# Kernel tuning notes

Measured on AMD Instinct MI355X. Metric: run time of the kernel, lower is better.

The kernel has to match this reference:

```python
import jax, jax.numpy as jnp
import numpy as np

N, M, B, C, L, H = 8192, 8192, 16, 512, 64, 8
HEAD_DIM = C // H
PER_BATCH_KEYS = M // B
MASK_VAL = -1000.0  # matches torch masked_fill_ value


def setup_inputs() -> dict:
    key0 = jax.random.key(0)
    ks = jax.random.split(key0, 8)
    query = jax.random.normal(ks[0], (N, C), jnp.float32)
    key = jax.random.normal(ks[1], (M, C), jnp.float32)
    value = jax.random.normal(ks[2], (M, C), jnp.float32)
    # xavier-ish init for projections
    in_proj_weight = jax.random.normal(ks[3], (3 * C, C), jnp.float32) * (1.0 / np.sqrt(C))
    in_proj_bias = jnp.zeros((3 * C,), jnp.float32)
    out_w = jax.random.normal(ks[4], (C, C), jnp.float32) * (1.0 / np.sqrt(C))
    out_b = jnp.zeros((C,), jnp.float32)
    index_pair = jax.random.randint(ks[5], (N, L), 0, PER_BATCH_KEYS).astype(jnp.int32)
    pad = jax.random.uniform(ks[6], (N, L)) < 0.05
    index_pair = jnp.where(pad, jnp.int32(-1), index_pair)
    query_batch_cnt = jnp.full((B,), N // B, jnp.int32)
    key_batch_cnt = jnp.full((B,), PER_BATCH_KEYS, jnp.int32)
    index_pair_batch = jnp.repeat(jnp.arange(B, dtype=jnp.int32), N // B)
    return {
        "query": query, "key": key, "value": value,
        "in_proj_weight": in_proj_weight, "in_proj_bias": in_proj_bias,
        "out_w": out_w, "out_b": out_b,
        "index_pair": index_pair, "query_batch_cnt": query_batch_cnt,
        "key_batch_cnt": key_batch_cnt, "index_pair_batch": index_pair_batch,
    }


def reference(query, key, value, in_proj_weight, in_proj_bias, out_w, out_b,
              index_pair, query_batch_cnt, key_batch_cnt, index_pair_batch):
    embed_dim = query.shape[-1]
    scaling = float(HEAD_DIM) ** -0.5
    # qkv projections (in_proj_weight is [3C, C], applied as F.linear => x @ W.T + b)
    q = (query @ in_proj_weight[:embed_dim].T + in_proj_bias[:embed_dim]) * scaling
    k = key @ in_proj_weight[embed_dim:2 * embed_dim].T + in_proj_bias[embed_dim:2 * embed_dim]
    v = value @ in_proj_weight[2 * embed_dim:].T + in_proj_bias[2 * embed_dim:]
    q = q.reshape(N, H, HEAD_DIM)
    k = k.reshape(M, H, HEAD_DIM)
    v = v.reshape(M, H, HEAD_DIM)
    # local -> global key indices: offset by start of each query's batch key block
    key_start = jnp.cumsum(key_batch_cnt) - key_batch_cnt          # (B,)
    offset = key_start[index_pair_batch]                            # (N,)
    valid = index_pair >= 0                                         # (N, L)
    gidx = jnp.where(valid, index_pair + offset[:, None], 0)        # (N, L), safe gather
    # gather-based scores: (N, L, H)
    scores = jnp.einsum("nhd,nlhd->nlh", q, k[gidx])
    scores = jnp.where(valid[..., None], scores, MASK_VAL)
    w = jax.nn.softmax(scores, axis=1)                              # softmax over neighbors L
    # weighted value sum; masked weights underflow to exactly 0 in fp32
    attn = jnp.einsum("nlh,nlhd->nhd", w, v[gidx]).reshape(N, embed_dim)
    attn = attn @ out_w.T + out_b
    return attn, w.sum(axis=-1) / H
```

## Files before the change

kernel.cpp:

```cpp
#include <hip/hip_runtime.h>
#include <hip/hip_bf16.h>
#include <math.h>

#define NQ 8192
#define MK 8192
#define CD 512
#define LN 64
#define HH 8
#define HD 64
#define BB 16

typedef short short8 __attribute__((ext_vector_type(8)));
typedef float floatx4 __attribute__((ext_vector_type(4)));

__device__ __forceinline__ unsigned short f2bf(float x) {
    unsigned int u = __builtin_bit_cast(unsigned int, x);
    return (unsigned short)((u + 0x7FFFu + ((u >> 16) & 1u)) >> 16);
}
__device__ __forceinline__ unsigned int pkbf(float lo, float hi) {
    float2 f; f.x = lo; f.y = hi;
    __hip_bfloat162 h2 = __float22bfloat162_rn(f);
    unsigned int u;
    __builtin_memcpy(&u, &h2, 4);
    return u;
}
__device__ __forceinline__ float bflo(unsigned int u) {
    return __builtin_bit_cast(float, u << 16);
}
__device__ __forceinline__ float bfhij(unsigned int u) {
    return __builtin_bit_cast(float, u);
}
__device__ __forceinline__ short8 u4s8(uint4 u) {
    short8 s; __builtin_memcpy(&s, &u, 16); return s;
}

__device__ __forceinline__ void gl_lds16(const unsigned short* g, unsigned short* l) {
    __builtin_amdgcn_global_load_lds(
        (const __attribute__((address_space(1))) unsigned int*)g,
        (__attribute__((address_space(3))) unsigned int*)l, 16, 0, 0);
}

struct ConvSeg { const float* src; unsigned short* dst; int n4; };
struct ConvArgs { ConvSeg s[5]; };

__global__ __launch_bounds__(256) void convert_bf16(ConvArgs a) {
    const int seg = blockIdx.y;
    const int i = blockIdx.x * 256 + threadIdx.x;
    if (i >= a.s[seg].n4) return;
    const float4 v = ((const float4*)a.s[seg].src)[i];
    uint2 o; o.x = pkbf(v.x, v.y); o.y = pkbf(v.z, v.w);
    ((uint2*)a.s[seg].dst)[i] = o;
}

__device__ __forceinline__ void gemm_bf_body(const unsigned short* __restrict__ A,
                                             const unsigned short* __restrict__ W,
                                             const float* __restrict__ bias,
                                             float* __restrict__ outf,
                                             unsigned short* __restrict__ outb,
                                             float scale) {
    __shared__ unsigned short As[64 * 64];
    __shared__ unsigned short Bs[128 * 64];

    const int tid  = threadIdx.x;
    const int row0 = blockIdx.x * 64;
    const int col0 = blockIdx.y * 128;

    const int w    = tid >> 6;
    const int lane = tid & 63;
    const int q    = lane >> 4;
    const int ml   = lane & 15;

    const int sr = lane >> 3;
    const int sg = (lane & 7) ^ sr;
    const unsigned short* Ap = A + (size_t)(row0 + w * 16 + sr) * CD + sg * 8;
    const unsigned short* Wp = W + (size_t)(col0 + w * 32 + sr) * CD + sg * 8;
    unsigned short* Asw = &As[(w * 16) * 64];
    unsigned short* Bsw = &Bs[(w * 32) * 64];

    floatx4 acc[4][2];
#pragma unroll
    for (int i = 0; i < 4; ++i)
#pragma unroll
        for (int j = 0; j < 2; ++j)
            acc[i][j] = (floatx4){0.f, 0.f, 0.f, 0.f};

    for (int k0 = 0; k0 < CD; k0 += 64) {
        __syncthreads();
#pragma unroll
        for (int i = 0; i < 2; ++i)
            gl_lds16(Ap + (size_t)(i * 8) * CD + k0, Asw + i * 8 * 64);
#pragma unroll
        for (int i = 0; i < 4; ++i)
            gl_lds16(Wp + (size_t)(i * 8) * CD + k0, Bsw + i * 8 * 64);
        __syncthreads();

#pragma unroll
        for (int kw = 0; kw < 2; ++kw) {
            short8 af[4], bf[2];
            const int gp = ((kw * 4 + q) ^ (ml & 7)) * 8;
#pragma unroll
            for (int mi = 0; mi < 4; ++mi)
                af[mi] = *(const short8*)&As[(mi * 16 + ml) * 64 + gp];
#pragma unroll
            for (int ni = 0; ni < 2; ++ni)
                bf[ni] = *(const short8*)&Bs[(w * 32 + ni * 16 + ml) * 64 + gp];
#pragma unroll
            for (int mi = 0; mi < 4; ++mi)
#pragma unroll
                for (int ni = 0; ni < 2; ++ni)
                    acc[mi][ni] = __builtin_amdgcn_mfma_f32_16x16x32_bf16(
                        af[mi], bf[ni], acc[mi][ni], 0, 0, 0);
        }
    }

    float bv[2];
#pragma unroll
    for (int ni = 0; ni < 2; ++ni)
        bv[ni] = bias[col0 + w * 32 + ni * 16 + ml];
#pragma unroll
    for (int mi = 0; mi < 4; ++mi) {
#pragma unroll
        for (int ni = 0; ni < 2; ++ni) {
            const int cg = col0 + w * 32 + ni * 16 + ml;
#pragma unroll
            for (int rr = 0; rr < 4; ++rr) {
                const int rg = row0 + mi * 16 + q * 4 + rr;
                const float val = (acc[mi][ni][rr] + bv[ni]) * scale;
                if (outb) outb[(size_t)rg * CD + cg] = f2bf(val);
                else      outf[(size_t)rg * CD + cg] = val;
            }
        }
    }
}

__global__ __launch_bounds__(256) void qkv_gemm(const unsigned short* __restrict__ A_bf,
                                                const unsigned short* __restrict__ w_bf,
                                                const float* __restrict__ bias,
                                                unsigned short* __restrict__ q_bf,
                                                unsigned short* __restrict__ k_bf,
                                                unsigned short* __restrict__ v_bf) {
    const int z = blockIdx.z;
    const unsigned short* A = A_bf + (size_t)z * NQ * CD;
    unsigned short* outb = (z == 0) ? q_bf : ((z == 1) ? k_bf : v_bf);
    gemm_bf_body(A, w_bf + (size_t)z * CD * CD, bias + (size_t)z * CD,
                 nullptr, outb, (z == 0) ? 0.125f : 1.0f);
}

__global__ __launch_bounds__(256) void out_gemm(const unsigned short* __restrict__ A,
                                                const unsigned short* __restrict__ W,
                                                const float* __restrict__ bias,
                                                float* __restrict__ out) {
    gemm_bf_body(A, W, bias, out, nullptr, 1.0f);
}

__global__ __launch_bounds__(256) void attn_kernel(
    const unsigned short* __restrict__ q_bf,
    const unsigned short* __restrict__ k_bf,
    const unsigned short* __restrict__ v_bf,
    const int* __restrict__ index_pair,
    const int* __restrict__ key_batch_cnt,
    const int* __restrict__ index_pair_batch,
    unsigned short* __restrict__ attn_bf,
    float* __restrict__ out2) {
    const int tid  = threadIdx.x;
    const int wid  = tid >> 6;
    const int lane = tid & 63;
    const int bx   = blockIdx.x;
    const int n    = (bx & 7) * (NQ / 8) + (bx >> 3) * 4 + wid;

    const int quad = lane >> 4;
    const int ml   = lane & 15;
    const int r    = lane >> 3;
    const int dg   = lane & 7;

    __shared__ float sc_s[4][LN];
    float* sc = sc_s[wid];

    int cnt = (lane < BB) ? key_batch_cnt[lane] : 0;
#pragma unroll
    for (int d = 1; d < BB; d <<= 1) {
        const int t = __shfl_up(cnt, d, 64);
        if (lane >= d) cnt += t;
    }
    const int batch = index_pair_batch[n];
    const int off0  = (batch > 0) ? __shfl(cnt, batch - 1, 64) : 0;

    const int gi = index_pair[n * LN + lane];
    const unsigned long long vmask = __ballot(gi >= 0);
    const int g = (gi >= 0) ? (gi + off0) : 0;

    int krow[4];
#pragma unroll
    for (int grp = 0; grp < 4; ++grp)
        krow[grp] = __shfl(g, grp * 16 + ml, 64);
    int vrow[8];
#pragma unroll
    for (int it = 0; it < 8; ++it)
        vrow[it] = __shfl(g, it * 8 + r, 64);

    const size_t qbase = (size_t)n * CD;
    float s8 = 0.f;

    for (int h = 0; h < HH; ++h) {
        const char* qp = (const char*)(q_bf + qbase + h * HD) + quad * 16;
        const uint4 bq0 = *(const uint4*)qp;
        const uint4 bq1 = *(const uint4*)(qp + 64);
        uint4 a0[4], a1[4];
#pragma unroll
        for (int grp = 0; grp < 4; ++grp) {
            const char* kp = (const char*)(k_bf + (size_t)krow[grp] * CD + h * HD) + quad * 16;
            a0[grp] = *(const uint4*)kp;
            a1[grp] = *(const uint4*)(kp + 64);
        }
        uint4 vv[8];
#pragma unroll
        for (int it = 0; it < 8; ++it) {
            const char* vp = (const char*)(v_bf + (size_t)vrow[it] * CD + h * HD) + dg * 16;
            vv[it] = *(const uint4*)vp;
        }

#pragma unroll
        for (int grp = 0; grp < 4; ++grp) {
            floatx4 sa = (floatx4){0.f, 0.f, 0.f, 0.f};
            sa = __builtin_amdgcn_mfma_f32_16x16x32_bf16(u4s8(a0[grp]), u4s8(bq0), sa, 0, 0, 0);
            sa = __builtin_amdgcn_mfma_f32_16x16x32_bf16(u4s8(a1[grp]), u4s8(bq1), sa, 0, 0, 0);
            if (ml == 0) {
#pragma unroll
                for (int rr = 0; rr < 4; ++rr) sc[grp * 16 + quad * 4 + rr] = sa[rr];
            }
        }

        float score = sc[lane];
        if (!((vmask >> lane) & 1ull)) score = -1000.0f;
        float mx = score;
#pragma unroll
        for (int o = 32; o > 0; o >>= 1) mx = fmaxf(mx, __shfl_xor(mx, o, 64));
        float e = __expf(score - mx);
        float s = e;
#pragma unroll
        for (int o = 32; o > 0; o >>= 1) s += __shfl_xor(s, o, 64);
        const float w = e / s;
        s8 += w;

        float a8[8] = {0.f, 0.f, 0.f, 0.f, 0.f, 0.f, 0.f, 0.f};
#pragma unroll
        for (int it = 0; it < 8; ++it) {
            const float wl = __shfl(w, it * 8 + r, 64);
            a8[0] = fmaf(wl, bflo(vv[it].x),  a8[0]);
            a8[1] = fmaf(wl, bfhij(vv[it].x), a8[1]);
            a8[2] = fmaf(wl, bflo(vv[it].y),  a8[2]);
            a8[3] = fmaf(wl, bfhij(vv[it].y), a8[3]);
            a8[4] = fmaf(wl, bflo(vv[it].z),  a8[4]);
            a8[5] = fmaf(wl, bfhij(vv[it].z), a8[5]);
            a8[6] = fmaf(wl, bflo(vv[it].w),  a8[6]);
            a8[7] = fmaf(wl, bfhij(vv[it].w), a8[7]);
        }
#pragma unroll
        for (int o = 8; o <= 32; o <<= 1)
#pragma unroll
            for (int d = 0; d < 8; ++d) a8[d] += __shfl_xor(a8[d], o, 64);
        attn_bf[qbase + h * HD + dg * 8 + r] = f2bf(a8[r]);
    }

    out2[(size_t)n * LN + lane] = s8 * (1.0f / HH);
}

extern "C" void kernel_launch(void* const* d_in, const int* in_sizes, int n_in,
                              void* d_out, int out_size, void* d_ws, size_t ws_size,
                              hipStream_t stream) {
    const float* query   = (const float*)d_in[0];
    const float* key     = (const float*)d_in[1];
    const float* value   = (const float*)d_in[2];
    const float* ipw     = (const float*)d_in[3];
    const float* ipb     = (const float*)d_in[4];
    const float* out_w   = (const float*)d_in[5];
    const float* out_b   = (const float*)d_in[6];
    const int*   index_pair       = (const int*)d_in[7];
    const int*   key_batch_cnt    = (const int*)d_in[9];
    const int*   index_pair_batch = (const int*)d_in[10];

    float* out = (float*)d_out;
    unsigned short* q_bf  = (unsigned short*)d_ws;
    unsigned short* k_bf  = q_bf + (size_t)NQ * CD;
    unsigned short* v_bf  = k_bf + (size_t)NQ * CD;
    unsigned short* A_bf  = v_bf + (size_t)NQ * CD;
    unsigned short* w_bf  = A_bf + (size_t)3 * NQ * CD;
    unsigned short* ow_bf = w_bf + (size_t)3 * CD * CD;
    unsigned short* attn_bf = A_bf;

    ConvArgs ca;
    ca.s[0] = {query, A_bf,                       NQ * CD / 4};
    ca.s[1] = {key,   A_bf + (size_t)NQ * CD,     NQ * CD / 4};
    ca.s[2] = {value, A_bf + (size_t)2 * NQ * CD, NQ * CD / 4};
    ca.s[3] = {ipw,   w_bf,                       3 * CD * CD / 4};
    ca.s[4] = {out_w, ow_bf,                      CD * CD / 4};
    dim3 g0(NQ * CD / 4 / 256, 5);
    convert_bf16<<<g0, 256, 0, stream>>>(ca);

    dim3 g1(NQ / 64, CD / 128, 3);
    qkv_gemm<<<g1, 256, 0, stream>>>(A_bf, w_bf, ipb, q_bf, k_bf, v_bf);

    attn_kernel<<<NQ / 4, 256, 0, stream>>>(q_bf, k_bf, v_bf, index_pair,
                                            key_batch_cnt, index_pair_batch,
                                            attn_bf, out + (size_t)NQ * CD);

    dim3 g3(NQ / 64, CD / 128, 1);
    out_gemm<<<g3, 256, 0, stream>>>(attn_bf, ow_bf, out_b, out);
}
```

Before: 221.0 us.

## Restructure gather attention: register softmax, prefetch K across heads, row-wise V

Folds log2(e) into the Q projection scale so the softmax can use raw v_exp_f32 and v_rcp_f32. The softmax now runs on MFMA output registers with only two cross-lane shuffles instead of an LDS round trip plus 64-lane butterfly reductions. K and Q loads for the next head are double-buffered. The value pass is rewritten to gather full 1 KB V rows per neighbor, reading the weights from LDS, which removes the per-head shuffle reductions of the accumulator and emits one 16-byte store per lane. The cost is more registers and an LDS weight buffer, plus a slight precision change from bf16 Q carrying the log2(e) factor.

```diff
diff --git a/kernel.cpp b/kernel.cpp
--- a/kernel.cpp
+++ b/kernel.cpp
@@ -32,6 +32,12 @@
 }
 __device__ __forceinline__ short8 u4s8(uint4 u) {
     short8 s; __builtin_memcpy(&s, &u, 16); return s;
+}
+__device__ __forceinline__ float exp2v(float x) {
+    float r; asm("v_exp_f32 %0, %1" : "=v"(r) : "v"(x)); return r;
+}
+__device__ __forceinline__ float rcpv(float x) {
+    float r; asm("v_rcp_f32 %0, %1" : "=v"(r) : "v"(x)); return r;
 }
 
 __device__ __forceinline__ void gl_lds16(const unsigned short* g, unsigned short* l) {
@@ -132,6 +138,8 @@
         }
     }
 }
+
+#define QSCALE 0.18033688011112042f
 
 __global__ __launch_bounds__(256) void qkv_gemm(const unsigned short* __restrict__ A_bf,
                                                 const unsigned short* __restrict__ w_bf,
@@ -143,7 +151,7 @@
     const unsigned short* A = A_bf + (size_t)z * NQ * CD;
     unsigned short* outb = (z == 0) ? q_bf : ((z == 1) ? k_bf : v_bf);
     gemm_bf_body(A, w_bf + (size_t)z * CD * CD, bias + (size_t)z * CD,
-                 nullptr, outb, (z == 0) ? 0.125f : 1.0f);
+                 nullptr, outb, (z == 0) ? QSCALE : 1.0f);
 }
 
 __global__ __launch_bounds__(256) void out_gemm(const unsigned short* __restrict__ A,
@@ -151,6 +159,17 @@
                                                 const float* __restrict__ bias,
                                                 float* __restrict__ out) {
     gemm_bf_body(A, W, bias, out, nullptr, 1.0f);
+}
+
+__device__ __forceinline__ void fma8(float (&a)[8], uint4 u, float w) {
+    a[0] = fmaf(w, bflo(u.x),  a[0]);
+    a[1] = fmaf(w, bfhij(u.x), a[1]);
+    a[2] = fmaf(w, bflo(u.y),  a[2]);
+    a[3] = fmaf(w, bfhij(u.y), a[3]);
+    a[4] = fmaf(w, bflo(u.z),  a[4]);
+    a[5] = fmaf(w, bfhij(u.z), a[5]);
+    a[6] = fmaf(w, bflo(u.w),  a[6]);
+    a[7] = fmaf(w, bfhij(u.w), a[7]);
 }
 
 __global__ __launch_bounds__(256) void attn_kernel(
@@ -170,11 +189,9 @@
 
     const int quad = lane >> 4;
     const int ml   = lane & 15;
-    const int r    = lane >> 3;
-    const int dg   = lane & 7;
-
-    __shared__ float sc_s[4][LN];
-    float* sc = sc_s[wid];
+
+    __shared__ float w_s[4][HH][68];
+    float* ws = &w_s[wid][0][0];
 
     int cnt = (lane < BB) ? key_batch_cnt[lane] : 0;
 #pragma unroll
@@ -193,75 +210,131 @@
 #pragma unroll
     for (int grp = 0; grp < 4; ++grp)
         krow[grp] = __shfl(g, grp * 16 + ml, 64);
-    int vrow[8];
-#pragma unroll
-    for (int it = 0; it < 8; ++it)
-        vrow[it] = __shfl(g, it * 8 + r, 64);
-
-    const size_t qbase = (size_t)n * CD;
+
+    const unsigned long long tb = vmask >> (quad * 4);
+    const unsigned mybits =
+        (unsigned)( (tb & 0xFull)
+                  | (((tb >> 16) & 0xFull) << 4)
+                  | (((tb >> 32) & 0xFull) << 8)
+                  | (((tb >> 48) & 0xFull) << 12));
+    bool bc[16];
+#pragma unroll
+    for (int i = 0; i < 16; ++i) bc[i] = (mybits >> i) & 1u;
+    const bool p0 = ml & 1, p1 = ml & 2, p2 = ml & 4, p3 = ml & 8;
+    const int jpub = (ml >> 2) * 16 + quad * 4 + (ml & 3);
+
+    const char* qp = (const char*)(q_bf + (size_t)n * CD) + quad * 16;
+    const char* kp[4];
+#pragma unroll
+    for (int grp = 0; grp < 4; ++grp)
+        kp[grp] = (const char*)(k_bf + (size_t)krow[grp] * CD) + quad * 16;
+
+    uint4 ka[2][8], qa[2][2];
+#pragma unroll
+    for (int grp = 0; grp < 4; ++grp) {
+        ka[0][grp * 2]     = *(const uint4*)(kp[grp]);
+        ka[0][grp * 2 + 1] = *(const uint4*)(kp[grp] + 64);
+    }
+    qa[0][0] = *(const uint4*)(qp);
+    qa[0][1] = *(const uint4*)(qp + 64);
+
+#pragma unroll
+    for (int h = 0; h < HH; ++h) {
+        const int cb = h & 1;
+        if (h < HH - 1) {
+#pragma unroll
+            for (int grp = 0; grp < 4; ++grp) {
+                ka[cb ^ 1][grp * 2]     = *(const uint4*)(kp[grp] + (h + 1) * 128);
+                ka[cb ^ 1][grp * 2 + 1] = *(const uint4*)(kp[grp] + (h + 1) * 128 + 64);
+            }
+            qa[cb ^ 1][0] = *(const uint4*)(qp + (h + 1) * 128);
+            qa[cb ^ 1][1] = *(const uint4*)(qp + (h + 1) * 128 + 64);
+        }
+
+        floatx4 sa[4];
+#pragma unroll
+        for (int grp = 0; grp < 4; ++grp) {
+            floatx4 z = (floatx4){0.f, 0.f, 0.f, 0.f};
+            z = __builtin_amdgcn_mfma_f32_16x16x32_bf16(u4s8(ka[cb][grp * 2]),
+                                                        u4s8(qa[cb][0]), z, 0, 0, 0);
+            z = __builtin_amdgcn_mfma_f32_16x16x32_bf16(u4s8(ka[cb][grp * 2 + 1]),
+                                                        u4s8(qa[cb][1]), z, 0, 0, 0);
+            sa[grp] = z;
+        }
+
+        float sc[16];
+#pragma unroll
+        for (int grp = 0; grp < 4; ++grp)
+#pragma unroll
+            for (int rr = 0; rr < 4; ++rr)
+                sc[grp * 4 + rr] = bc[grp * 4 + rr] ? sa[grp][rr] : -1000.0f;
+
+        float m8[8];
+#pragma unroll
+        for (int i = 0; i < 8; ++i) m8[i] = fmaxf(sc[2 * i], sc[2 * i + 1]);
+        float mx = fmaxf(fmaxf(fmaxf(m8[0], m8[1]), fmaxf(m8[2], m8[3])),
+                         fmaxf(fmaxf(m8[4], m8[5]), fmaxf(m8[6], m8[7])));
+        mx = fmaxf(mx, __shfl_xor(mx, 16, 64));
+        mx = fmaxf(mx, __shfl_xor(mx, 32, 64));
+
+        float e[16];
+#pragma unroll
+        for (int i = 0; i < 16; ++i) e[i] = exp2v(sc[i] - mx);
+        float s4[8];
+#pragma unroll
+        for (int i = 0; i < 8; ++i) s4[i] = e[2 * i] + e[2 * i + 1];
+        float s = ((s4[0] + s4[1]) + (s4[2] + s4[3])) + ((s4[4] + s4[5]) + (s4[6] + s4[7]));
+        s += __shfl_xor(s, 16, 64);
+        s += __shfl_xor(s, 32, 64);
+        const float rs = rcpv(s);
+
+        float t4[4];
+#pragma unroll
+        for (int gsel = 0; gsel < 4; ++gsel) {
+            const float e01 = p0 ? e[gsel * 4 + 1] : e[gsel * 4 + 0];
+            const float e23 = p0 ? e[gsel * 4 + 3] : e[gsel * 4 + 2];
+            t4[gsel] = p1 ? e23 : e01;
+        }
+        const float u0 = p2 ? t4[1] : t4[0];
+        const float u1 = p2 ? t4[3] : t4[2];
+        const float pick = p3 ? u1 : u0;
+        ws[h * 68 + jpub] = pick * rs;
+    }
+
+    float acc[8] = {0.f, 0.f, 0.f, 0.f, 0.f, 0.f, 0.f, 0.f};
+    const float* wrow = ws + (lane >> 3) * 68;
+    uint4 vr[2][8];
+#pragma unroll
+    for (int i = 0; i < 8; ++i) {
+        const int row = __builtin_amdgcn_readlane(g, i);
+        vr[0][i] = *(const uint4*)(v_bf + (size_t)row * CD + (lane << 3));
+    }
+#pragma unroll
+    for (int c = 0; c < 8; ++c) {
+        const int cb = c & 1;
+        if (c < 7) {
+#pragma unroll
+            for (int i = 0; i < 8; ++i) {
+                const int row = __builtin_amdgcn_readlane(g, (c + 1) * 8 + i);
+                vr[cb ^ 1][i] = *(const uint4*)(v_bf + (size_t)row * CD + (lane << 3));
+            }
+        }
+        const float4 w0 = *(const float4*)(wrow + c * 8);
+        const float4 w1 = *(const float4*)(wrow + c * 8 + 4);
+        fma8(acc, vr[cb][0], w0.x); fma8(acc, vr[cb][1], w0.y);
+        fma8(acc, vr[cb][2], w0.z); fma8(acc, vr[cb][3], w0.w);
+        fma8(acc, vr[cb][4], w1.x); fma8(acc, vr[cb][5], w1.y);
+        fma8(acc, vr[cb][6], w1.z); fma8(acc, vr[cb][7], w1.w);
+    }
+
+    uint4 o;
+    o.x = pkbf(acc[0], acc[1]); o.y = pkbf(acc[2], acc[3]);
+    o.z = pkbf(acc[4], acc[5]); o.w = pkbf(acc[6], acc[7]);
+    *(uint4*)(attn_bf + (size_t)n * CD + (lane << 3)) = o;
+
     float s8 = 0.f;
-
-    for (int h = 0; h < HH; ++h) {
-        const char* qp = (const char*)(q_bf + qbase + h * HD) + quad * 16;
-        const uint4 bq0 = *(const uint4*)qp;
-        const uint4 bq1 = *(const uint4*)(qp + 64);
-        uint4 a0[4], a1[4];
-#pragma unroll
-        for (int grp = 0; grp < 4; ++grp) {
-            const char* kp = (const char*)(k_bf + (size_t)krow[grp] * CD + h * HD) + quad * 16;
-            a0[grp] = *(const uint4*)kp;
-            a1[grp] = *(const uint4*)(kp + 64);
-        }
-        uint4 vv[8];
-#pragma unroll
-        for (int it = 0; it < 8; ++it) {
-            const char* vp = (const char*)(v_bf + (size_t)vrow[it] * CD + h * HD) + dg * 16;
-            vv[it] = *(const uint4*)vp;
-        }
-
-#pragma unroll
-        for (int grp = 0; grp < 4; ++grp) {
-            floatx4 sa = (floatx4){0.f, 0.f, 0.f, 0.f};
-            sa = __builtin_amdgcn_mfma_f32_16x16x32_bf16(u4s8(a0[grp]), u4s8(bq0), sa, 0, 0, 0);
-            sa = __builtin_amdgcn_mfma_f32_16x16x32_bf16(u4s8(a1[grp]), u4s8(bq1), sa, 0, 0, 0);
-            if (ml == 0) {
-#pragma unroll
-                for (int rr = 0; rr < 4; ++rr) sc[grp * 16 + quad * 4 + rr] = sa[rr];
-            }
-        }
-
-        float score = sc[lane];
-        if (!((vmask >> lane) & 1ull)) score = -1000.0f;
-        float mx = score;
-#pragma unroll
-        for (int o = 32; o > 0; o >>= 1) mx = fmaxf(mx, __shfl_xor(mx, o, 64));
-        float e = __expf(score - mx);
-        float s = e;
-#pragma unroll
-        for (int o = 32; o > 0; o >>= 1) s += __shfl_xor(s, o, 64);
-        const float w = e / s;
-        s8 += w;
-
-        float a8[8] = {0.f, 0.f, 0.f, 0.f, 0.f, 0.f, 0.f, 0.f};
-#pragma unroll
-        for (int it = 0; it < 8; ++it) {
-            const float wl = __shfl(w, it * 8 + r, 64);
-            a8[0] = fmaf(wl, bflo(vv[it].x),  a8[0]);
-            a8[1] = fmaf(wl, bfhij(vv[it].x), a8[1]);
-            a8[2] = fmaf(wl, bflo(vv[it].y),  a8[2]);
-            a8[3] = fmaf(wl, bfhij(vv[it].y), a8[3]);
-            a8[4] = fmaf(wl, bflo(vv[it].z),  a8[4]);
-            a8[5] = fmaf(wl, bfhij(vv[it].z), a8[5]);
-            a8[6] = fmaf(wl, bflo(vv[it].w),  a8[6]);
-            a8[7] = fmaf(wl, bfhij(vv[it].w), a8[7]);
-        }
-#pragma unroll
-        for (int o = 8; o <= 32; o <<= 1)
-#pragma unroll
-            for (int d = 0; d < 8; ++d) a8[d] += __shfl_xor(a8[d], o, 64);
-        attn_bf[qbase + h * HD + dg * 8 + r] = f2bf(a8[r]);
-    }
-
+#pragma unroll
+    for (int h = 0; h < HH; ++h) s8 += ws[h * 68 + lane];
     out2[(size_t)n * LN + lane] = s8 * (1.0f / HH);
 }
 
```

Result: slower. 245.2 us (+10.9%).

## Restructure sparse attention kernel: register softmax, double-buffered loads, full-row V accumulation

Applied to the files above, without the earlier changes.

The attention kernel now keeps the MFMA score results in registers and does the softmax with quad-level shuffles instead of round-tripping scores through shared memory with 6-step full-wave reductions. K/Q loads for the next head are double-buffered against the current head's compute. The value pass is reorganised so each lane owns 8 contiguous output channels across all heads and reads weights from LDS, which removes the per-head cross-lane shuffle reduction. Exponentials use raw v_exp_f32 with log2(e) folded into the Q scale, and division becomes v_rcp_f32. The trade-off is much higher register pressure, which the launch bound of 3 waves per SIMD must accommodate, plus slightly lower precision in exp and reciprocal.

```diff
diff --git a/kernel.cpp b/kernel.cpp
--- a/kernel.cpp
+++ b/kernel.cpp
@@ -32,6 +32,12 @@
 }
 __device__ __forceinline__ short8 u4s8(uint4 u) {
     short8 s; __builtin_memcpy(&s, &u, 16); return s;
+}
+__device__ __forceinline__ float exp2v(float x) {
+    float r; asm("v_exp_f32 %0, %1" : "=v"(r) : "v"(x)); return r;
+}
+__device__ __forceinline__ float rcpv(float x) {
+    float r; asm("v_rcp_f32 %0, %1" : "=v"(r) : "v"(x)); return r;
 }
 
 __device__ __forceinline__ void gl_lds16(const unsigned short* g, unsigned short* l) {
@@ -132,6 +138,8 @@
         }
     }
 }
+
+#define QSCALE 0.18033688011112042f
 
 __global__ __launch_bounds__(256) void qkv_gemm(const unsigned short* __restrict__ A_bf,
                                                 const unsigned short* __restrict__ w_bf,
@@ -143,7 +151,7 @@
     const unsigned short* A = A_bf + (size_t)z * NQ * CD;
     unsigned short* outb = (z == 0) ? q_bf : ((z == 1) ? k_bf : v_bf);
     gemm_bf_body(A, w_bf + (size_t)z * CD * CD, bias + (size_t)z * CD,
-                 nullptr, outb, (z == 0) ? 0.125f : 1.0f);
+                 nullptr, outb, (z == 0) ? QSCALE : 1.0f);
 }
 
 __global__ __launch_bounds__(256) void out_gemm(const unsigned short* __restrict__ A,
@@ -153,7 +161,95 @@
     gemm_bf_body(A, W, bias, out, nullptr, 1.0f);
 }
 
-__global__ __launch_bounds__(256) void attn_kernel(
+#define MFMA16(a, b, c) __builtin_amdgcn_mfma_f32_16x16x32_bf16(a, b, c, 0, 0, 0)
+#define MK_ -1000.0f
+
+
+#define KA_LOAD(S, h) do {                                                    \
+    S##0 = *(const uint4*)(kp0 + (h) * 128);                                  \
+    S##1 = *(const uint4*)(kp0 + (h) * 128 + 64);                             \
+    S##2 = *(const uint4*)(kp1 + (h) * 128);                                  \
+    S##3 = *(const uint4*)(kp1 + (h) * 128 + 64);                             \
+    S##4 = *(const uint4*)(kp2 + (h) * 128);                                  \
+    S##5 = *(const uint4*)(kp2 + (h) * 128 + 64);                             \
+    S##6 = *(const uint4*)(kp3 + (h) * 128);                                  \
+    S##7 = *(const uint4*)(kp3 + (h) * 128 + 64);                             \
+    S##q0 = *(const uint4*)(qp + (h) * 128);                                  \
+    S##q1 = *(const uint4*)(qp + (h) * 128 + 64);                             \
+} while (0)
+
+#define HEAD_COMPUTE(S, h) do {                                               \
+    floatx4 z0 = (floatx4){0.f,0.f,0.f,0.f}, z1 = z0, z2 = z0, z3 = z0;       \
+    z0 = MFMA16(u4s8(S##0), u4s8(S##q0), z0);                                 \
+    z0 = MFMA16(u4s8(S##1), u4s8(S##q1), z0);                                 \
+    z1 = MFMA16(u4s8(S##2), u4s8(S##q0), z1);                                 \
+    z1 = MFMA16(u4s8(S##3), u4s8(S##q1), z1);                                 \
+    z2 = MFMA16(u4s8(S##4), u4s8(S##q0), z2);                                 \
+    z2 = MFMA16(u4s8(S##5), u4s8(S##q1), z2);                                 \
+    z3 = MFMA16(u4s8(S##6), u4s8(S##q0), z3);                                 \
+    z3 = MFMA16(u4s8(S##7), u4s8(S##q1), z3);                                 \
+    float s00 = b0  ? z0[0] : MK_,  s01 = b1  ? z0[1] : MK_;                  \
+    float s02 = b2  ? z0[2] : MK_,  s03 = b3  ? z0[3] : MK_;                  \
+    float s04 = b4  ? z1[0] : MK_,  s05 = b5  ? z1[1] : MK_;                  \
+    float s06 = b6  ? z1[2] : MK_,  s07 = b7  ? z1[3] : MK_;                  \
+    float s08 = b8  ? z2[0] : MK_,  s09 = b9  ? z2[1] : MK_;                  \
+    float s10 = b10 ? z2[2] : MK_,  s11 = b11 ? z2[3] : MK_;                  \
+    float s12 = b12 ? z3[0] : MK_,  s13 = b13 ? z3[1] : MK_;                  \
+    float s14 = b14 ? z3[2] : MK_,  s15 = b15 ? z3[3] : MK_;                  \
+    float mx = fmaxf(fmaxf(fmaxf(fmaxf(s00, s01), fmaxf(s02, s03)),          \
+                           fmaxf(fmaxf(s04, s05), fmaxf(s06, s07))),         \
+                     fmaxf(fmaxf(fmaxf(s08, s09), fmaxf(s10, s11)),          \
+                           fmaxf(fmaxf(s12, s13), fmaxf(s14, s15))));        \
+    mx = fmaxf(mx, __shfl_xor(mx, 16, 64));                                   \
+    mx = fmaxf(mx, __shfl_xor(mx, 32, 64));                                   \
+    s00 = exp2v(s00 - mx); s01 = exp2v(s01 - mx);                             \
+    s02 = exp2v(s02 - mx); s03 = exp2v(s03 - mx);                             \
+    s04 = exp2v(s04 - mx); s05 = exp2v(s05 - mx);                             \
+    s06 = exp2v(s06 - mx); s07 = exp2v(s07 - mx);                             \
+    s08 = exp2v(s08 - mx); s09 = exp2v(s09 - mx);                             \
+    s10 = exp2v(s10 - mx); s11 = exp2v(s11 - mx);                             \
+    s12 = exp2v(s12 - mx); s13 = exp2v(s13 - mx);                             \
+    s14 = exp2v(s14 - mx); s15 = exp2v(s15 - mx);                             \
+    float sm = (((s00 + s01) + (s02 + s03)) + ((s04 + s05) + (s06 + s07)))    \
+             + (((s08 + s09) + (s10 + s11)) + ((s12 + s13) + (s14 + s15)));   \
+    sm += __shfl_xor(sm, 16, 64);                                             \
+    sm += __shfl_xor(sm, 32, 64);                                             \
+    const float rs = rcpv(sm);                                                \
+    const float t0 = p1 ? (p0 ? s03 : s02) : (p0 ? s01 : s00);                \
+    const float t1 = p1 ? (p0 ? s07 : s06) : (p0 ? s05 : s04);                \
+    const float t2 = p1 ? (p0 ? s11 : s10) : (p0 ? s09 : s08);                \
+    const float t3 = p1 ? (p0 ? s15 : s14) : (p0 ? s13 : s12);                \
+    const float pick = p3 ? (p2 ? t3 : t2) : (p2 ? t1 : t0);                  \
+    ws[(h) * 68 + jpub] = pick * rs;                                          \
+} while (0)
+
+#define V_LOAD(S, c) do {                                                     \
+    S##0 = *(const uint4*)(v_bf + (size_t)__builtin_amdgcn_readlane(g, (c) * 8 + 0) * CD + dco); \
+    S##1 = *(const uint4*)(v_bf + (size_t)__builtin_amdgcn_readlane(g, (c) * 8 + 1) * CD + dco); \
+    S##2 = *(const uint4*)(v_bf + (size_t)__builtin_amdgcn_readlane(g, (c) * 8 + 2) * CD + dco); \
+    S##3 = *(const uint4*)(v_bf + (size_t)__builtin_amdgcn_readlane(g, (c) * 8 + 3) * CD + dco); \
+    S##4 = *(const uint4*)(v_bf + (size_t)__builtin_amdgcn_readlane(g, (c) * 8 + 4) * CD + dco); \
+    S##5 = *(const uint4*)(v_bf + (size_t)__builtin_amdgcn_readlane(g, (c) * 8 + 5) * CD + dco); \
+    S##6 = *(const uint4*)(v_bf + (size_t)__builtin_amdgcn_readlane(g, (c) * 8 + 6) * CD + dco); \
+    S##7 = *(const uint4*)(v_bf + (size_t)__builtin_amdgcn_readlane(g, (c) * 8 + 7) * CD + dco); \
+} while (0)
+
+#define FMA8(u, wgt) do {                                                     \
+    const float w_ = (wgt);                                                   \
+    a0 = fmaf(w_, bflo((u).x),  a0);  a1 = fmaf(w_, bfhij((u).x), a1);        \
+    a2 = fmaf(w_, bflo((u).y),  a2);  a3 = fmaf(w_, bfhij((u).y), a3);        \
+    a4 = fmaf(w_, bflo((u).z),  a4);  a5 = fmaf(w_, bfhij((u).z), a5);        \
+    a6 = fmaf(w_, bflo((u).w),  a6);  a7 = fmaf(w_, bfhij((u).w), a7);        \
+} while (0)
+
+#define V_CONS(S, c) do {                                                     \
+    const float4 w0 = *(const float4*)(wrow + (c) * 8);                       \
+    const float4 w1 = *(const float4*)(wrow + (c) * 8 + 4);                   \
+    FMA8(S##0, w0.x); FMA8(S##1, w0.y); FMA8(S##2, w0.z); FMA8(S##3, w0.w);   \
+    FMA8(S##4, w1.x); FMA8(S##5, w1.y); FMA8(S##6, w1.z); FMA8(S##7, w1.w);   \
+} while (0)
+
+__global__ __launch_bounds__(256, 3) void attn_kernel(
     const unsigned short* __restrict__ q_bf,
     const unsigned short* __restrict__ k_bf,
     const unsigned short* __restrict__ v_bf,
@@ -170,11 +266,9 @@
 
     const int quad = lane >> 4;
     const int ml   = lane & 15;
-    const int r    = lane >> 3;
-    const int dg   = lane & 7;
-
-    __shared__ float sc_s[4][LN];
-    float* sc = sc_s[wid];
+
+    __shared__ float w_s[4][HH][68];
+    float* ws = &w_s[wid][0][0];
 
     int cnt = (lane < BB) ? key_batch_cnt[lane] : 0;
 #pragma unroll
@@ -189,79 +283,72 @@
     const unsigned long long vmask = __ballot(gi >= 0);
     const int g = (gi >= 0) ? (gi + off0) : 0;
 
-    int krow[4];
-#pragma unroll
-    for (int grp = 0; grp < 4; ++grp)
-        krow[grp] = __shfl(g, grp * 16 + ml, 64);
-    int vrow[8];
-#pragma unroll
-    for (int it = 0; it < 8; ++it)
-        vrow[it] = __shfl(g, it * 8 + r, 64);
-
-    const size_t qbase = (size_t)n * CD;
+    const int krow0 = __shfl(g, 0 * 16 + ml, 64);
+    const int krow1 = __shfl(g, 1 * 16 + ml, 64);
+    const int krow2 = __shfl(g, 2 * 16 + ml, 64);
+    const int krow3 = __shfl(g, 3 * 16 + ml, 64);
+
+    const unsigned long long tb = vmask >> (quad * 4);
+    const unsigned mybits =
+        (unsigned)( (tb & 0xFull)
+                  | (((tb >> 16) & 0xFull) << 4)
+                  | (((tb >> 32) & 0xFull) << 8)
+                  | (((tb >> 48) & 0xFull) << 12));
+    const bool b0  = mybits & 1u,          b1  = (mybits >> 1) & 1u;
+    const bool b2  = (mybits >> 2) & 1u,   b3  = (mybits >> 3) & 1u;
+    const bool b4  = (mybits >> 4) & 1u,   b5  = (mybits >> 5) & 1u;
+    const bool b6  = (mybits >> 6) & 1u,   b7  = (mybits >> 7) & 1u;
+    const bool b8  = (mybits >> 8) & 1u,   b9  = (mybits >> 9) & 1u;
+    const bool b10 = (mybits >> 10) & 1u,  b11 = (mybits >> 11) & 1u;
+    const bool b12 = (mybits >> 12) & 1u,  b13 = (mybits >> 13) & 1u;
+    const bool b14 = (mybits >> 14) & 1u,  b15 = (mybits >> 15) & 1u;
+    const bool p0 = ml & 1, p1 = ml & 2, p2 = ml & 4, p3 = ml & 8;
+    const int jpub = (ml >> 2) * 16 + quad * 4 + (ml & 3);
+
+    const char* qp  = (const char*)(q_bf + (size_t)n * CD) + quad * 16;
+    const char* kp0 = (const char*)(k_bf + (size_t)krow0 * CD) + quad * 16;
+    const char* kp1 = (const char*)(k_bf + (size_t)krow1 * CD) + quad * 16;
+    const char* kp2 = (const char*)(k_bf + (size_t)krow2 * CD) + quad * 16;
+    const char* kp3 = (const char*)(k_bf + (size_t)krow3 * CD) + quad * 16;
+
+    uint4 kaA0, kaA1, kaA2, kaA3, kaA4, kaA5, kaA6, kaA7, kaAq0, kaAq1;
+    uint4 kaB0, kaB1, kaB2, kaB3, kaB4, kaB5, kaB6, kaB7, kaBq0, kaBq1;
+
+    KA_LOAD(kaA, 0);
+#pragma unroll
+    for (int hp = 0; hp < HH; hp += 2) {
+        KA_LOAD(kaB, hp + 1);
+        HEAD_COMPUTE(kaA, hp);
+        if (hp + 2 < HH) KA_LOAD(kaA, hp + 2);
+        HEAD_COMPUTE(kaB, hp + 1);
+    }
+
+    float a0 = 0.f, a1 = 0.f, a2 = 0.f, a3 = 0.f;
+    float a4 = 0.f, a5 = 0.f, a6 = 0.f, a7 = 0.f;
+    const float* wrow = ws + (lane >> 3) * 68;
+    const int dco = lane << 3;
+
+    uint4 vA0, vA1, vA2, vA3, vA4, vA5, vA6, vA7;
+    uint4 vB0, vB1, vB2, vB3, vB4, vB5, vB6, vB7;
+
+    V_LOAD(vA, 0);
+    V_LOAD(vB, 1);  V_CONS(vA, 0);
+    V_LOAD(vA, 2);  V_CONS(vB, 1);
+    V_LOAD(vB, 3);  V_CONS(vA, 2);
+    V_LOAD(vA, 4);  V_CONS(vB, 3);
+    V_LOAD(vB, 5);  V_CONS(vA, 4);
+    V_LOAD(vA, 6);  V_CONS(vB, 5);
+    V_LOAD(vB, 7);  V_CONS(vA, 6);
+    V_CONS(vB, 7);
+
+    uint4 o;
+    o.x = pkbf(a0, a1); o.y = pkbf(a2, a3);
+    o.z = pkbf(a4, a5); o.w = pkbf(a6, a7);
+    *(uint4*)(attn_bf + (size_t)n * CD + dco) = o;
+
     float s8 = 0.f;
-
-    for (int h = 0; h < HH; ++h) {
-        const char* qp = (const char*)(q_bf + qbase + h * HD) + quad * 16;
-        const uint4 bq0 = *(const uint4*)qp;
-        const uint4 bq1 = *(const uint4*)(qp + 64);
-        uint4 a0[4], a1[4];
-#pragma unroll
-        for (int grp = 0; grp < 4; ++grp) {
-            const char* kp = (const char*)(k_bf + (size_t)krow[grp] * CD + h * HD) + quad * 16;
-            a0[grp] = *(const uint4*)kp;
-            a1[grp] = *(const uint4*)(kp + 64);
-        }
-        uint4 vv[8];
-#pragma unroll
-        for (int it = 0; it < 8; ++it) {
-            const char* vp = (const char*)(v_bf + (size_t)vrow[it] * CD + h * HD) + dg * 16;
-            vv[it] = *(const uint4*)vp;
-        }
-
-#pragma unroll
-        for (int grp = 0; grp < 4; ++grp) {
-            floatx4 sa = (floatx4){0.f, 0.f, 0.f, 0.f};
-            sa = __builtin_amdgcn_mfma_f32_16x16x32_bf16(u4s8(a0[grp]), u4s8(bq0), sa, 0, 0, 0);
-            sa = __builtin_amdgcn_mfma_f32_16x16x32_bf16(u4s8(a1[grp]), u4s8(bq1), sa, 0, 0, 0);
-            if (ml == 0) {
-#pragma unroll
-                for (int rr = 0; rr < 4; ++rr) sc[grp * 16 + quad * 4 + rr] = sa[rr];
-            }
-        }
-
-        float score = sc[lane];
-        if (!((vmask >> lane) & 1ull)) score = -1000.0f;
-        float mx = score;
-#pragma unroll
-        for (int o = 32; o > 0; o >>= 1) mx = fmaxf(mx, __shfl_xor(mx, o, 64));
-        float e = __expf(score - mx);
-        float s = e;
-#pragma unroll
-        for (int o = 32; o > 0; o >>= 1) s += __shfl_xor(s, o, 64);
-        const float w = e / s;
-        s8 += w;
-
-        float a8[8] = {0.f, 0.f, 0.f, 0.f, 0.f, 0.f, 0.f, 0.f};
-#pragma unroll
-        for (int it = 0; it < 8; ++it) {
-            const float wl = __shfl(w, it * 8 + r, 64);
-            a8[0] = fmaf(wl, bflo(vv[it].x),  a8[0]);
-            a8[1] = fmaf(wl, bfhij(vv[it].x), a8[1]);
-            a8[2] = fmaf(wl, bflo(vv[it].y),  a8[2]);
-            a8[3] = fmaf(wl, bfhij(vv[it].y), a8[3]);
-            a8[4] = fmaf(wl, bflo(vv[it].z),  a8[4]);
-            a8[5] = fmaf(wl, bfhij(vv[it].z), a8[5]);
-            a8[6] = fmaf(wl, bflo(vv[it].w),  a8[6]);
-            a8[7] = fmaf(wl, bfhij(vv[it].w), a8[7]);
-        }
-#pragma unroll
-        for (int o = 8; o <= 32; o <<= 1)
-#pragma unroll
-            for (int d = 0; d < 8; ++d) a8[d] += __shfl_xor(a8[d], o, 64);
-        attn_bf[qbase + h * HD + dg * 8 + r] = f2bf(a8[r]);
-    }
-
+#pragma unroll
+    for (int h = 0; h < HH; ++h) s8 += ws[h * 68 + lane];
     out2[(size_t)n * LN + lane] = s8 * (1.0f / HH);
 }
 
```

Result: slower. 225.7 us (+2.1%).

## Stage per-batch-head K/V tiles in LDS and restructure attention per (batch, head)

Applied to the files above, without the earlier changes.

The attention kernel now assigns each block one (batch, head) pair and a tile of 128 queries. It loads that batch's 512 keys and values for the head into swizzled LDS, so the gathers read shared memory rather than scattered global rows. Softmax uses raw v_exp_f32 and v_rcp_f32, with log2(e) folded into the Q scale. A per-head weight buffer plus a separate reduce kernel produces the head-averaged weights. This cuts redundant global gather traffic but assumes fixed 512 queries and keys per batch and adds an extra kernel and a workspace round-trip.

```diff
diff --git a/kernel.cpp b/kernel.cpp
--- a/kernel.cpp
+++ b/kernel.cpp
@@ -9,6 +9,8 @@
 #define HH 8
 #define HD 64
 #define BB 16
+#define KPB 512
+#define QPB 512
 
 typedef short short8 __attribute__((ext_vector_type(8)));
 typedef float floatx4 __attribute__((ext_vector_type(4)));
@@ -32,6 +34,12 @@
 }
 __device__ __forceinline__ short8 u4s8(uint4 u) {
     short8 s; __builtin_memcpy(&s, &u, 16); return s;
+}
+__device__ __forceinline__ float exp2v(float x) {
+    float r; asm("v_exp_f32 %0, %1" : "=v"(r) : "v"(x)); return r;
+}
+__device__ __forceinline__ float rcpv(float x) {
+    float r; asm("v_rcp_f32 %0, %1" : "=v"(r) : "v"(x)); return r;
 }
 
 __device__ __forceinline__ void gl_lds16(const unsigned short* g, unsigned short* l) {
@@ -132,6 +140,8 @@
         }
     }
 }
+
+#define QSCALE 0.18033688011112042f
 
 __global__ __launch_bounds__(256) void qkv_gemm(const unsigned short* __restrict__ A_bf,
                                                 const unsigned short* __restrict__ w_bf,
@@ -143,7 +153,7 @@
     const unsigned short* A = A_bf + (size_t)z * NQ * CD;
     unsigned short* outb = (z == 0) ? q_bf : ((z == 1) ? k_bf : v_bf);
     gemm_bf_body(A, w_bf + (size_t)z * CD * CD, bias + (size_t)z * CD,
-                 nullptr, outb, (z == 0) ? 0.125f : 1.0f);
+                 nullptr, outb, (z == 0) ? QSCALE : 1.0f);
 }
 
 __global__ __launch_bounds__(256) void out_gemm(const unsigned short* __restrict__ A,
@@ -153,28 +163,45 @@
     gemm_bf_body(A, W, bias, out, nullptr, 1.0f);
 }
 
-__global__ __launch_bounds__(256) void attn_kernel(
+#define MFMA16(a, b, c) __builtin_amdgcn_mfma_f32_16x16x32_bf16(a, b, c, 0, 0, 0)
+#define MK_ -1000.0f
+
+
+#define FMA8(u, wgt) do {                                                     \
+    const float w_ = (wgt);                                                   \
+    a0 = fmaf(w_, bflo((u).x),  a0);  a1 = fmaf(w_, bfhij((u).x), a1);        \
+    a2 = fmaf(w_, bflo((u).y),  a2);  a3 = fmaf(w_, bfhij((u).y), a3);        \
+    a4 = fmaf(w_, bflo((u).z),  a4);  a5 = fmaf(w_, bfhij((u).z), a5);        \
+    a6 = fmaf(w_, bflo((u).w),  a6);  a7 = fmaf(w_, bfhij((u).w), a7);        \
+} while (0)
+
+#define KRD(row, ch) (*(const uint4*)&K_s[(row) * 64 + ((((ch) ^ ((row) & 7))) * 8)])
+
+__global__ __launch_bounds__(512, 2) void attn_kernel(
     const unsigned short* __restrict__ q_bf,
     const unsigned short* __restrict__ k_bf,
     const unsigned short* __restrict__ v_bf,
     const int* __restrict__ index_pair,
     const int* __restrict__ key_batch_cnt,
-    const int* __restrict__ index_pair_batch,
     unsigned short* __restrict__ attn_bf,
-    float* __restrict__ out2) {
+    float* __restrict__ W8) {
     const int tid  = threadIdx.x;
     const int wid  = tid >> 6;
     const int lane = tid & 63;
-    const int bx   = blockIdx.x;
-    const int n    = (bx & 7) * (NQ / 8) + (bx >> 3) * 4 + wid;
-
-    const int quad = lane >> 4;
-    const int ml   = lane & 15;
-    const int r    = lane >> 3;
-    const int dg   = lane & 7;
-
-    __shared__ float sc_s[4][LN];
-    float* sc = sc_s[wid];
+    const int bid  = blockIdx.x;
+    const int pair = bid & 127;
+    const int qt   = bid >> 7;
+    const int head = pair & 7;
+    const int batch= pair >> 3;
+
+    const int quad = lane >> 4, ml = lane & 15;
+    const int r8 = lane >> 3, c8 = lane & 7;
+
+    __shared__ unsigned short K_s[KPB * 64];
+    __shared__ unsigned short V_s[KPB * 64];
+    __shared__ int   g_s[8 * 64];
+    __shared__ float w_st[8 * 64];
+    __shared__ float red_s[8 * 64 * 9];
 
     int cnt = (lane < BB) ? key_batch_cnt[lane] : 0;
 #pragma unroll
@@ -182,87 +209,151 @@
         const int t = __shfl_up(cnt, d, 64);
         if (lane >= d) cnt += t;
     }
-    const int batch = index_pair_batch[n];
-    const int off0  = (batch > 0) ? __shfl(cnt, batch - 1, 64) : 0;
-
-    const int gi = index_pair[n * LN + lane];
-    const unsigned long long vmask = __ballot(gi >= 0);
-    const int g = (gi >= 0) ? (gi + off0) : 0;
-
-    int krow[4];
-#pragma unroll
-    for (int grp = 0; grp < 4; ++grp)
-        krow[grp] = __shfl(g, grp * 16 + ml, 64);
-    int vrow[8];
-#pragma unroll
-    for (int it = 0; it < 8; ++it)
-        vrow[it] = __shfl(g, it * 8 + r, 64);
-
-    const size_t qbase = (size_t)n * CD;
-    float s8 = 0.f;
-
-    for (int h = 0; h < HH; ++h) {
-        const char* qp = (const char*)(q_bf + qbase + h * HD) + quad * 16;
-        const uint4 bq0 = *(const uint4*)qp;
-        const uint4 bq1 = *(const uint4*)(qp + 64);
-        uint4 a0[4], a1[4];
-#pragma unroll
-        for (int grp = 0; grp < 4; ++grp) {
-            const char* kp = (const char*)(k_bf + (size_t)krow[grp] * CD + h * HD) + quad * 16;
-            a0[grp] = *(const uint4*)kp;
-            a1[grp] = *(const uint4*)(kp + 64);
-        }
-        uint4 vv[8];
-#pragma unroll
-        for (int it = 0; it < 8; ++it) {
-            const char* vp = (const char*)(v_bf + (size_t)vrow[it] * CD + h * HD) + dg * 16;
-            vv[it] = *(const uint4*)vp;
-        }
-
-#pragma unroll
-        for (int grp = 0; grp < 4; ++grp) {
-            floatx4 sa = (floatx4){0.f, 0.f, 0.f, 0.f};
-            sa = __builtin_amdgcn_mfma_f32_16x16x32_bf16(u4s8(a0[grp]), u4s8(bq0), sa, 0, 0, 0);
-            sa = __builtin_amdgcn_mfma_f32_16x16x32_bf16(u4s8(a1[grp]), u4s8(bq1), sa, 0, 0, 0);
-            if (ml == 0) {
-#pragma unroll
-                for (int rr = 0; rr < 4; ++rr) sc[grp * 16 + quad * 4 + rr] = sa[rr];
-            }
-        }
-
-        float score = sc[lane];
-        if (!((vmask >> lane) & 1ull)) score = -1000.0f;
-        float mx = score;
-#pragma unroll
-        for (int o = 32; o > 0; o >>= 1) mx = fmaxf(mx, __shfl_xor(mx, o, 64));
-        float e = __expf(score - mx);
-        float s = e;
-#pragma unroll
-        for (int o = 32; o > 0; o >>= 1) s += __shfl_xor(s, o, 64);
-        const float w = e / s;
-        s8 += w;
-
-        float a8[8] = {0.f, 0.f, 0.f, 0.f, 0.f, 0.f, 0.f, 0.f};
-#pragma unroll
-        for (int it = 0; it < 8; ++it) {
-            const float wl = __shfl(w, it * 8 + r, 64);
-            a8[0] = fmaf(wl, bflo(vv[it].x),  a8[0]);
-            a8[1] = fmaf(wl, bfhij(vv[it].x), a8[1]);
-            a8[2] = fmaf(wl, bflo(vv[it].y),  a8[2]);
-            a8[3] = fmaf(wl, bfhij(vv[it].y), a8[3]);
-            a8[4] = fmaf(wl, bflo(vv[it].z),  a8[4]);
-            a8[5] = fmaf(wl, bfhij(vv[it].z), a8[5]);
-            a8[6] = fmaf(wl, bflo(vv[it].w),  a8[6]);
-            a8[7] = fmaf(wl, bfhij(vv[it].w), a8[7]);
-        }
-#pragma unroll
-        for (int o = 8; o <= 32; o <<= 1)
-#pragma unroll
-            for (int d = 0; d < 8; ++d) a8[d] += __shfl_xor(a8[d], o, 64);
-        attn_bf[qbase + h * HD + dg * 8 + r] = f2bf(a8[r]);
+    const int off0 = (batch > 0) ? __shfl(cnt, batch - 1, 64) : 0;
+
+#pragma unroll
+    for (int j = 0; j < 8; ++j) {
+        const int rowb = wid * 64 + j * 8;
+        const size_t grow = (size_t)(off0 + rowb + r8);
+        gl_lds16(k_bf + grow * CD + head * HD + ((c8 ^ r8) * 8), &K_s[rowb * 64]);
+        gl_lds16(v_bf + grow * CD + head * HD + (c8 * 8),        &V_s[rowb * 64]);
     }
-
-    out2[(size_t)n * LN + lane] = s8 * (1.0f / HH);
+    __syncthreads();
+
+    const int n0 = batch * QPB + qt * 128 + wid * 16;
+    const bool p0 = ml & 1, p1 = ml & 2, p2 = ml & 4, p3 = ml & 8;
+    const int jpub = (ml >> 2) * 16 + quad * 4 + (ml & 3);
+    int*   gs  = &g_s[wid * 64];
+    float* wst = &w_st[wid * 64];
+    float* red = &red_s[wid * 64 * 9];
+
+    int idx = index_pair[(size_t)n0 * LN + lane];
+    for (int qi = 0; qi < 16; ++qi) {
+        const int n = n0 + qi;
+        const int idx_next = (qi < 15) ? index_pair[(size_t)(n + 1) * LN + lane] : 0;
+
+        const unsigned long long vmask = __ballot(idx >= 0);
+        const int g = (idx >= 0) ? idx : 0;
+        gs[lane] = g;
+
+        const int krow0 = __shfl(g, ml, 64);
+        const int krow1 = __shfl(g, 16 + ml, 64);
+        const int krow2 = __shfl(g, 32 + ml, 64);
+        const int krow3 = __shfl(g, 48 + ml, 64);
+
+        const unsigned long long tb = vmask >> (quad * 4);
+        const unsigned mybits =
+            (unsigned)( (tb & 0xFull)
+                      | (((tb >> 16) & 0xFull) << 4)
+                      | (((tb >> 32) & 0xFull) << 8)
+                      | (((tb >> 48) & 0xFull) << 12));
+        const bool b0  = mybits & 1u,          b1  = (mybits >> 1) & 1u;
+        const bool b2  = (mybits >> 2) & 1u,   b3  = (mybits >> 3) & 1u;
+        const bool b4  = (mybits >> 4) & 1u,   b5  = (mybits >> 5) & 1u;
+        const bool b6  = (mybits >> 6) & 1u,   b7  = (mybits >> 7) & 1u;
+        const bool b8  = (mybits >> 8) & 1u,   b9  = (mybits >> 9) & 1u;
+        const bool b10 = (mybits >> 10) & 1u,  b11 = (mybits >> 11) & 1u;
+        const bool b12 = (mybits >> 12) & 1u,  b13 = (mybits >> 13) & 1u;
+        const bool b14 = (mybits >> 14) & 1u,  b15 = (mybits >> 15) & 1u;
+
+        const unsigned short* qrow = q_bf + (size_t)n * CD + head * HD;
+        const uint4 qa0 = *(const uint4*)(qrow + quad * 8);
+        const uint4 qa1 = *(const uint4*)(qrow + 32 + quad * 8);
+
+        const uint4 kf00 = KRD(krow0, quad), kf01 = KRD(krow0, 4 + quad);
+        const uint4 kf10 = KRD(krow1, quad), kf11 = KRD(krow1, 4 + quad);
+        const uint4 kf20 = KRD(krow2, quad), kf21 = KRD(krow2, 4 + quad);
+        const uint4 kf30 = KRD(krow3, quad), kf31 = KRD(krow3, 4 + quad);
+
+        floatx4 z0 = (floatx4){0.f,0.f,0.f,0.f}, z1 = z0, z2 = z0, z3 = z0;
+        z0 = MFMA16(u4s8(kf00), u4s8(qa0), z0);
+        z0 = MFMA16(u4s8(kf01), u4s8(qa1), z0);
+        z1 = MFMA16(u4s8(kf10), u4s8(qa0), z1);
+        z1 = MFMA16(u4s8(kf11), u4s8(qa1), z1);
+        z2 = MFMA16(u4s8(kf20), u4s8(qa0), z2);
+        z2 = MFMA16(u4s8(kf21), u4s8(qa1), z2);
+        z3 = MFMA16(u4s8(kf30), u4s8(qa0), z3);
+        z3 = MFMA16(u4s8(kf31), u4s8(qa1), z3);
+
+        float s00 = b0  ? z0[0] : MK_,  s01 = b1  ? z0[1] : MK_;
+        float s02 = b2  ? z0[2] : MK_,  s03 = b3  ? z0[3] : MK_;
+        float s04 = b4  ? z1[0] : MK_,  s05 = b5  ? z1[1] : MK_;
+        float s06 = b6  ? z1[2] : MK_,  s07 = b7  ? z1[3] : MK_;
+        float s08 = b8  ? z2[0] : MK_,  s09 = b9  ? z2[1] : MK_;
+        float s10 = b10 ? z2[2] : MK_,  s11 = b11 ? z2[3] : MK_;
+        float s12 = b12 ? z3[0] : MK_,  s13 = b13 ? z3[1] : MK_;
+        float s14 = b14 ? z3[2] : MK_,  s15 = b15 ? z3[3] : MK_;
+        float mx = fmaxf(fmaxf(fmaxf(fmaxf(s00, s01), fmaxf(s02, s03)),
+                               fmaxf(fmaxf(s04, s05), fmaxf(s06, s07))),
+                         fmaxf(fmaxf(fmaxf(s08, s09), fmaxf(s10, s11)),
+                               fmaxf(fmaxf(s12, s13), fmaxf(s14, s15))));
+        mx = fmaxf(mx, __shfl_xor(mx, 16, 64));
+        mx = fmaxf(mx, __shfl_xor(mx, 32, 64));
+        s00 = exp2v(s00 - mx); s01 = exp2v(s01 - mx);
+        s02 = exp2v(s02 - mx); s03 = exp2v(s03 - mx);
+        s04 = exp2v(s04 - mx); s05 = exp2v(s05 - mx);
+        s06 = exp2v(s06 - mx); s07 = exp2v(s07 - mx);
+        s08 = exp2v(s08 - mx); s09 = exp2v(s09 - mx);
+        s10 = exp2v(s10 - mx); s11 = exp2v(s11 - mx);
+        s12 = exp2v(s12 - mx); s13 = exp2v(s13 - mx);
+        s14 = exp2v(s14 - mx); s15 = exp2v(s15 - mx);
+        float sm = (((s00 + s01) + (s02 + s03)) + ((s04 + s05) + (s06 + s07)))
+                 + (((s08 + s09) + (s10 + s11)) + ((s12 + s13) + (s14 + s15)));
+        sm += __shfl_xor(sm, 16, 64);
+        sm += __shfl_xor(sm, 32, 64);
+        const float rs = rcpv(sm);
+        const float t0 = p1 ? (p0 ? s03 : s02) : (p0 ? s01 : s00);
+        const float t1 = p1 ? (p0 ? s07 : s06) : (p0 ? s05 : s04);
+        const float t2 = p1 ? (p0 ? s11 : s10) : (p0 ? s09 : s08);
+        const float t3 = p1 ? (p0 ? s15 : s14) : (p0 ? s13 : s12);
+        const float pick = p3 ? (p2 ? t3 : t2) : (p2 ? t1 : t0);
+        const float w = pick * rs;
+        wst[jpub] = w;
+        W8[((size_t)head * NQ + n) * LN + jpub] = w * 0.125f;
+
+        const int   vr0 = gs[0 * 8 + r8], vr1 = gs[1 * 8 + r8];
+        const int   vr2 = gs[2 * 8 + r8], vr3 = gs[3 * 8 + r8];
+        const int   vr4 = gs[4 * 8 + r8], vr5 = gs[5 * 8 + r8];
+        const int   vr6 = gs[6 * 8 + r8], vr7 = gs[7 * 8 + r8];
+        const float wv0 = wst[0 * 8 + r8], wv1 = wst[1 * 8 + r8];
+        const float wv2 = wst[2 * 8 + r8], wv3 = wst[3 * 8 + r8];
+        const float wv4 = wst[4 * 8 + r8], wv5 = wst[5 * 8 + r8];
+        const float wv6 = wst[6 * 8 + r8], wv7 = wst[7 * 8 + r8];
+        const uint4 vv0 = *(const uint4*)&V_s[vr0 * 64 + c8 * 8];
+        const uint4 vv1 = *(const uint4*)&V_s[vr1 * 64 + c8 * 8];
+        const uint4 vv2 = *(const uint4*)&V_s[vr2 * 64 + c8 * 8];
+        const uint4 vv3 = *(const uint4*)&V_s[vr3 * 64 + c8 * 8];
+        const uint4 vv4 = *(const uint4*)&V_s[vr4 * 64 + c8 * 8];
+        const uint4 vv5 = *(const uint4*)&V_s[vr5 * 64 + c8 * 8];
+        const uint4 vv6 = *(const uint4*)&V_s[vr6 * 64 + c8 * 8];
+        const uint4 vv7 = *(const uint4*)&V_s[vr7 * 64 + c8 * 8];
+        float a0 = 0.f, a1 = 0.f, a2 = 0.f, a3 = 0.f;
+        float a4 = 0.f, a5 = 0.f, a6 = 0.f, a7 = 0.f;
+        FMA8(vv0, wv0); FMA8(vv1, wv1); FMA8(vv2, wv2); FMA8(vv3, wv3);
+        FMA8(vv4, wv4); FMA8(vv5, wv5); FMA8(vv6, wv6); FMA8(vv7, wv7);
+
+        red[lane * 9 + 0] = a0; red[lane * 9 + 1] = a1;
+        red[lane * 9 + 2] = a2; red[lane * 9 + 3] = a3;
+        red[lane * 9 + 4] = a4; red[lane * 9 + 5] = a5;
+        red[lane * 9 + 6] = a6; red[lane * 9 + 7] = a7;
+        const int bcol = lane >> 3, e = lane & 7;
+        const float s = (((red[(0 * 8 + bcol) * 9 + e] + red[(1 * 8 + bcol) * 9 + e])
+                        + (red[(2 * 8 + bcol) * 9 + e] + red[(3 * 8 + bcol) * 9 + e]))
+                       + ((red[(4 * 8 + bcol) * 9 + e] + red[(5 * 8 + bcol) * 9 + e])
+                        + (red[(6 * 8 + bcol) * 9 + e] + red[(7 * 8 + bcol) * 9 + e])));
+        attn_bf[(size_t)n * CD + head * HD + lane] = f2bf(s);
+
+        idx = idx_next;
+    }
+}
+
+__global__ __launch_bounds__(256) void out2_reduce(const float* __restrict__ W8,
+                                                   float* __restrict__ out2) {
+    const size_t i = (size_t)blockIdx.x * 256 + threadIdx.x;
+    float s = 0.f;
+#pragma unroll
+    for (int h = 0; h < HH; ++h) s += W8[(size_t)h * NQ * LN + i];
+    out2[i] = s;
 }
 
 extern "C" void kernel_launch(void* const* d_in, const int* in_sizes, int n_in,
@@ -277,7 +368,6 @@
     const float* out_b   = (const float*)d_in[6];
     const int*   index_pair       = (const int*)d_in[7];
     const int*   key_batch_cnt    = (const int*)d_in[9];
-    const int*   index_pair_batch = (const int*)d_in[10];
 
     float* out = (float*)d_out;
     unsigned short* q_bf  = (unsigned short*)d_ws;
@@ -287,6 +377,7 @@
     unsigned short* w_bf  = A_bf + (size_t)3 * NQ * CD;
     unsigned short* ow_bf = w_bf + (size_t)3 * CD * CD;
     unsigned short* attn_bf = A_bf;
+    float* W8 = (float*)(A_bf + (size_t)NQ * CD);
 
     ConvArgs ca;
     ca.s[0] = {query, A_bf,                       NQ * CD / 4};
@@ -300,9 +391,10 @@
     dim3 g1(NQ / 64, CD / 128, 3);
     qkv_gemm<<<g1, 256, 0, stream>>>(A_bf, w_bf, ipb, q_bf, k_bf, v_bf);
 
-    attn_kernel<<<NQ / 4, 256, 0, stream>>>(q_bf, k_bf, v_bf, index_pair,
-                                            key_batch_cnt, index_pair_batch,
-                                            attn_bf, out + (size_t)NQ * CD);
+    attn_kernel<<<512, 512, 0, stream>>>(q_bf, k_bf, v_bf, index_pair,
+                                         key_batch_cnt, attn_bf, W8);
+
+    out2_reduce<<<NQ * LN / 256, 256, 0, stream>>>(W8, out + (size_t)NQ * CD);
 
     dim3 g3(NQ / 64, CD / 128, 1);
     out_gemm<<<g3, 256, 0, stream>>>(attn_bf, ow_bf, out_b, out);
```

Measured after the change: 208.3 us. 5.7% less time.
